# Optimization experiments

Hardware: AMD Instinct MI355X
Metric: run time of the kernel (lower is better)

## Reference

```python
import jax, jax.numpy as jnp
import numpy as np

K_TOP = 2  # top-k experts per token


def setup_inputs() -> dict:
    key = jax.random.key(0)
    k1, k2, k3 = jax.random.split(key, 3)
    B, S, H, E = 4, 2048, 1024, 8
    hidden_states = jax.random.normal(k1, (B, S, H), dtype=jnp.float32)
    router_w = jax.random.normal(k2, (E, H), dtype=jnp.float32) * 0.02
    expert_weights = jax.random.normal(k3, (E, H, H), dtype=jnp.float32) * 0.02
    return {"hidden_states": hidden_states, "router_w": router_w, "expert_weights": expert_weights}


def reference(hidden_states, router_w, expert_weights):
    B, S, H = hidden_states.shape
    x = hidden_states.reshape(-1, H)                      # [N, H], N = B*S
    logits = x @ router_w.T                               # [N, E]
    probs = jax.nn.softmax(logits, axis=-1)               # [N, E]
    topk_vals, topk_idx = jax.lax.top_k(probs, K_TOP)     # [N, K]
    topk_w = topk_vals / (topk_vals.sum(-1, keepdims=True) + 1e-6)  # [N, K]

    # Dense per-expert GEMM over all tokens (single-device dispatch = identity)
    expert_out = jnp.einsum('nh,eho->eno', x, expert_weights)  # [E, N, H]

    # all_to_all_combine: gather each token's K expert outputs
    combined = jnp.take_along_axis(
        expert_out.transpose(1, 0, 2),                    # [N, E, H]
        topk_idx[:, :, None], axis=1)                     # [N, K, H]
    combined = combined.transpose(1, 0, 2)                # [K, N, H]

    # remap bias: sum over last dim of one-hot(topk_idx) * router_prob == gathered prob
    remap_bias = jnp.take_along_axis(probs, topk_idx, axis=1).T[:, :, None]  # [K, N, 1]

    weights = topk_w.T[:, :, None]                        # [K, N, 1]
    out = ((combined + remap_bias) * weights).sum(axis=0) # [N, H]
    return out.reshape(B, S, H)
```

## Files before the change

kernel.cpp:

```cpp
#include <hip/hip_runtime.h>
#include <hip/hip_fp16.h>
#include <cstdint>

typedef unsigned short u16;
typedef __attribute__((ext_vector_type(8))) short short8;
typedef __attribute__((ext_vector_type(4))) float float4v;

#define NTOK 8192
#define HDIM 1024
#define NEXP 8
#define HTILE (128 * 64)
#define NITF 8
#define MAXT256 72
#define FATT 64
#define TMT 128
#define BKT 32
#define NITT (HDIM / BKT)
#define LAT (TMT * BKT)
#define WBLK 2048
#define RBLK 2048

__device__ __forceinline__ u16 f2bf(float f) {
    union { float f; uint32_t u; } v; v.f = f;
    uint32_t u = v.u;
    return (u16)((u + 0x7FFFu + ((u >> 16) & 1u)) >> 16);
}

__device__ __forceinline__ void gll16(const u16* g, u16* l) {
    __builtin_amdgcn_global_load_lds(
        (const __attribute__((address_space(1))) uint32_t*)g,
        (__attribute__((address_space(3))) uint32_t*)l,
        16, 0, 0);
}

__global__ __launch_bounds__(256) void prep(const float* __restrict__ x,
                                            const float* __restrict__ rw,
                                            const float* __restrict__ ew,
                                            u16* __restrict__ x_bf,
                                            u16* __restrict__ w_bf,
                                            float* __restrict__ wt0,
                                            float* __restrict__ wt1,
                                            float* __restrict__ biasv,
                                            int* __restrict__ sel,
                                            int* __restrict__ ctrl) {
    if (blockIdx.x == 0 && threadIdx.x < 132) ctrl[threadIdx.x] = 0;

    if (blockIdx.x < WBLK) {
        __shared__ float tile[64][65];
        const int bid = blockIdx.x;
        const int e  = bid >> 8;
        const int k0 = ((bid >> 4) & 15) * 64;
        const int n0 = (bid & 15) * 64;
        const int kr = threadIdx.x >> 2;
        const int ng = (threadIdx.x & 3) * 16;
        const float* src = ew + ((size_t)e << 20) + (size_t)(k0 + kr) * HDIM + n0 + ng;
#pragma unroll
        for (int j = 0; j < 4; j++) {
            const float4 v = *(const float4*)(src + 4 * j);
            tile[kr][ng + 4*j]     = v.x;
            tile[kr][ng + 4*j + 1] = v.y;
            tile[kr][ng + 4*j + 2] = v.z;
            tile[kr][ng + 4*j + 3] = v.w;
        }
        __syncthreads();
        const int nr = threadIdx.x >> 2;
        const int kg = (threadIdx.x & 3) * 16;
        u16* dst = w_bf + ((size_t)e << 20) + (size_t)(n0 + nr) * HDIM + k0 + kg;
#pragma unroll
        for (int j = 0; j < 4; j++) {
            ushort4 o;
            o.x = f2bf(tile[kg + 4*j][nr]);
            o.y = f2bf(tile[kg + 4*j + 1][nr]);
            o.z = f2bf(tile[kg + 4*j + 2][nr]);
            o.w = f2bf(tile[kg + 4*j + 3][nr]);
            *(ushort4*)(dst + 4 * j) = o;
        }
    } else {
        const int wv = threadIdx.x >> 6;
        const int l  = threadIdx.x & 63;
        const int n  = (blockIdx.x - WBLK) * 4 + wv;
        const float4* xr = (const float4*)(x + (size_t)n * HDIM);
        ushort4* xo = (ushort4*)(x_bf + (size_t)n * HDIM);

        float4 xv[4];
#pragma unroll
        for (int t = 0; t < 4; t++) {
            xv[t] = xr[t * 64 + l];
            ushort4 p;
            p.x = f2bf(xv[t].x); p.y = f2bf(xv[t].y);
            p.z = f2bf(xv[t].z); p.w = f2bf(xv[t].w);
            xo[t * 64 + l] = p;
        }

        float logits[NEXP];
#pragma unroll
        for (int e = 0; e < NEXP; e++) {
            const float4* rwe = (const float4*)(rw + e * HDIM);
            float acc = 0.f;
#pragma unroll
            for (int t = 0; t < 4; t++) {
                const float4 r = rwe[t * 64 + l];
                acc += xv[t].x * r.x + xv[t].y * r.y + xv[t].z * r.z + xv[t].w * r.w;
            }
#pragma unroll
            for (int s = 32; s > 0; s >>= 1) acc += __shfl_xor(acc, s, 64);
            logits[e] = acc;
        }

        if (l == 0) {
            float mx = logits[0];
#pragma unroll
            for (int e = 1; e < NEXP; e++) mx = fmaxf(mx, logits[e]);
            float p[NEXP]; float sum = 0.f;
#pragma unroll
            for (int e = 0; e < NEXP; e++) { p[e] = expf(logits[e] - mx); sum += p[e]; }
            const float inv = 1.f / sum;
#pragma unroll
            for (int e = 0; e < NEXP; e++) p[e] *= inv;
            int e0 = 0;
#pragma unroll
            for (int e = 1; e < NEXP; e++) if (p[e] > p[e0]) e0 = e;
            int e1 = (e0 == 0) ? 1 : 0;
#pragma unroll
            for (int e = 0; e < NEXP; e++) if (e != e0 && p[e] > p[e1]) e1 = e;
            const float p0 = p[e0], p1 = p[e1];
            const float wsum = p0 + p1 + 1e-6f;
            const float w0 = p0 / wsum, w1 = p1 / wsum;
            wt0[n] = w0; wt1[n] = w1;
            biasv[n] = w0 * p0 + w1 * p1;
            sel[n] = e0 | (e1 << 8);
        }
    }
}

__global__ __launch_bounds__(256) void build_lists(const int* __restrict__ sel,
                                                   int* __restrict__ lists,
                                                   int* __restrict__ ctrl,
                                                   int* __restrict__ tmap,
                                                   int* __restrict__ tmap128) {
    const int n  = blockIdx.x * 256 + threadIdx.x;
    const int wv = threadIdx.x >> 6;
    const int l  = threadIdx.x & 63;
    const int s  = sel[n];
    const int e0 = s & 0xFF, e1 = s >> 8;
    __shared__ int wcnt[NEXP][4];
    __shared__ int ebase[NEXP];
    int pf0 = 0, pf1 = 0;
    const unsigned long long ltmask = (1ULL << l) - 1ULL;
#pragma unroll
    for (int e = 0; e < NEXP; e++) {
        const int slot = (e0 == e) ? 0 : ((e1 == e) ? 1 : -1);
        const unsigned long long bal = __ballot(slot >= 0);
        const int pf = __popcll(bal & ltmask);
        if (slot == 0) pf0 = pf;
        if (slot == 1) pf1 = pf;
        if (l == 0) wcnt[e][wv] = __popcll(bal);
    }
    __syncthreads();
    if (threadIdx.x < NEXP) {
        const int e = threadIdx.x;
        const int tot = wcnt[e][0] + wcnt[e][1] + wcnt[e][2] + wcnt[e][3];
        ebase[e] = atomicAdd(&ctrl[e * 16], tot);
    }
    __syncthreads();
    int off0 = ebase[e0], off1 = ebase[e1];
#pragma unroll
    for (int i = 0; i < 4; i++) {
        off0 += (i < wv) ? wcnt[e0][i] : 0;
        off1 += (i < wv) ? wcnt[e1][i] : 0;
    }
    lists[e0 * NTOK + off0 + pf0] = n;
    lists[e1 * NTOK + off1 + pf1] = n | 0x10000;

    __shared__ int lastflag;
    __threadfence();
    if (threadIdx.x == 0) lastflag = (atomicAdd(&ctrl[128], 1) == (int)gridDim.x - 1);
    __syncthreads();
    if (lastflag) {
        __shared__ int tbase[NEXP + 1];
        __shared__ int cnts[NEXP];
        if (threadIdx.x == 0) {
            int acc = 0;
            for (int e = 0; e < NEXP; e++) {
                tbase[e] = acc;
                cnts[e] = atomicAdd(&ctrl[e * 16], 0);
                acc += (cnts[e] + 255) / 256;
            }
            tbase[NEXP] = acc;
        }
        __syncthreads();
        for (int i = threadIdx.x; i < MAXT256; i += 256) {
            int v = -1;
#pragma unroll
            for (int e = 0; e < NEXP; e++)
                if (i >= tbase[e] && i < tbase[e + 1]) v = (e << 16) | (i - tbase[e]);
            tmap[i] = v;
        }
        if (threadIdx.x < 16) {
            const int j = threadIdx.x;
            const int i256 = FATT + (j >> 1);
            int v = -1;
            if (i256 < tbase[NEXP]) {
                int ve = 0;
#pragma unroll
                for (int e = 0; e < NEXP; e++)
                    if (i256 >= tbase[e] && i256 < tbase[e + 1]) ve = e;
                const int m256 = i256 - tbase[ve];
                const int m128 = m256 * 2 + (j & 1);
                if (m128 * 128 < cnts[ve]) v = (ve << 16) | m128;
            }
            tmap128[j] = v;
        }
    }
}

__global__ __launch_bounds__(512, 2) void moe_gemm_fat(const u16* __restrict__ x_bf,
                                                       const u16* __restrict__ wt_bf,
                                                       const int* __restrict__ lists,
                                                       const int* __restrict__ ctrl,
                                                       const int* __restrict__ tmap,
                                                       const float* __restrict__ wt0,
                                                       const float* __restrict__ wt1,
                                                       const float* __restrict__ biasv,
                                                       __half* __restrict__ stage0,
                                                       __half* __restrict__ stage1) {
    const int ent = tmap[blockIdx.x];
    if (ent < 0) return;
    const int e = ent >> 16;
    const int tile_m = (ent & 0xFFFF) * 256;
    const int cnt = ctrl[e * 16];
    const int tn = blockIdx.y * 256;

    __shared__ u16 lA[4 * HTILE];
    __shared__ u16 lB[4 * HTILE];
    __shared__ int   toks[256];
    __shared__ float wgt[256];
    __shared__ float bia[256];
    __shared__ int   slt[256];

    const int t  = threadIdx.x;
    const int wv = t >> 6;
    const int l  = t & 63;

    if (t < 256) {
        const int idx = tile_m + t;
        int tok = 0; float w = 0.f, b = 0.f; int sl = 0;
        if (idx < cnt) {
            const int entry = lists[e * NTOK + idx];
            tok = entry & 0xFFFF;
            sl = entry >> 16;
            w = sl ? wt1[tok] : wt0[tok];
            b = sl ? 0.f : biasv[tok];
        }
        toks[t] = tok; wgt[t] = w; bia[t] = b; slt[t] = sl;
    }
    __syncthreads();

    const u16* const wbase = wt_bf + ((size_t)e << 20);
    const u16* pA[2][2]; const u16* pB[2][2];
    int dst0, dst1;
    {
        const int s0 = (0 * 8 + wv) * 64 + l;
        const int s1 = (1 * 8 + wv) * 64 + l;
        const int r0 = s0 >> 3, r1 = s1 >> 3;
        const int g0s = (s0 & 7) ^ (r0 & 7);
        const int g1s = (s1 & 7) ^ (r1 & 7);
        dst0 = (0 * 8 + wv) * 512;
        dst1 = (1 * 8 + wv) * 512;
#pragma unroll
        for (int h = 0; h < 2; h++) {
            pA[0][h] = x_bf + (size_t)toks[h * 128 + r0] * HDIM + g0s * 8;
            pA[1][h] = x_bf + (size_t)toks[h * 128 + r1] * HDIM + g1s * 8;
            pB[0][h] = wbase + (size_t)(tn + h * 128 + r0) * HDIM + g0s * 8;
            pB[1][h] = wbase + (size_t)(tn + h * 128 + r1) * HDIM + g1s * 8;
        }
    }

#define STAGE_A(par, h, ktile) do { \
    gll16(pA[0][h] + (ktile) * 64, lA + (par) * 2 * HTILE + (h) * HTILE + dst0); \
    gll16(pA[1][h] + (ktile) * 64, lA + (par) * 2 * HTILE + (h) * HTILE + dst1); } while (0)
#define STAGE_B(par, h, ktile) do { \
    gll16(pB[0][h] + (ktile) * 64, lB + (par) * 2 * HTILE + (h) * HTILE + dst0); \
    gll16(pB[1][h] + (ktile) * 64, lB + (par) * 2 * HTILE + (h) * HTILE + dst1); } while (0)

    const int wm2 = wv >> 2;
    const int wn4 = wv & 3;
    const int fm = l & 15;
    const int fq = l >> 4;
    const int f7 = fm & 7;
    const int pg0 = ((0 + fq) ^ f7) * 8;
    const int pg1 = ((4 + fq) ^ f7) * 8;
    const int arow = fm * 64;
    const int brow = (wn4 & 1) * 4096 + fm * 64;
    const u16* const Abase = lA + wm2 * HTILE;
    const u16* const Bbase = lB + (wn4 >> 1) * HTILE;

    short8 afr[4][2];
    short8 bfr[2][2][2];

#define LDA_H(par, mq) do { \
    _Pragma("unroll") \
    for (int mfL = 0; mfL < 4; mfL++) { \
        afr[mfL][0] = *(const short8*)(Abase + (par) * 2 * HTILE + ((mq) * 4 + mfL) * 1024 + arow + pg0); \
        afr[mfL][1] = *(const short8*)(Abase + (par) * 2 * HTILE + ((mq) * 4 + mfL) * 1024 + arow + pg1); \
    } } while (0)
#define LDB_H(par, nq) do { \
    _Pragma("unroll") \
    for (int nfL = 0; nfL < 2; nfL++) { \
        bfr[nq][nfL][0] = *(const short8*)(Bbase + (par) * 2 * HTILE + ((nq) * 2 + nfL) * 1024 + brow + pg0); \
        bfr[nq][nfL][1] = *(const short8*)(Bbase + (par) * 2 * HTILE + ((nq) * 2 + nfL) * 1024 + brow + pg1); \
    } } while (0)

    float4v acc[8][4];
#pragma unroll
    for (int i = 0; i < 8; i++)
#pragma unroll
        for (int j = 0; j < 4; j++) { float4v z = {0.f, 0.f, 0.f, 0.f}; acc[i][j] = z; }

#define MFMA_Q(mq, nq) do { \
    __builtin_amdgcn_s_setprio(1); \
    _Pragma("unroll") \
    for (int ks = 0; ks < 2; ks++) \
    _Pragma("unroll") \
    for (int mfL = 0; mfL < 4; mfL++) \
    _Pragma("unroll") \
    for (int nfL = 0; nfL < 2; nfL++) \
        acc[(mq) * 4 + mfL][(nq) * 2 + nfL] = __builtin_amdgcn_mfma_f32_16x16x32_bf16( \
            afr[mfL][ks], bfr[nq][nfL][ks], acc[(mq) * 4 + mfL][(nq) * 2 + nfL], 0, 0, 0); \
    __builtin_amdgcn_s_setprio(0); } while (0)

#define BARx() __builtin_amdgcn_s_barrier()
#define LGKM0 do { asm volatile("s_waitcnt lgkmcnt(0)" ::: "memory"); \
                   __builtin_amdgcn_sched_barrier(0); } while (0)
#define VM2 asm volatile("s_waitcnt vmcnt(2)" ::: "memory")
#define VM0 asm volatile("s_waitcnt vmcnt(0)" ::: "memory")

    STAGE_A(0, 0, 0); STAGE_A(0, 1, 0);
    STAGE_B(0, 0, 0); STAGE_B(0, 1, 0);
    STAGE_A(1, 0, 1);
    VM0; BARx();

#pragma unroll
    for (int it = 0; it < NITF; ++it) {
        const bool st = (it < NITF - 1);
        LDA_H(0, 0); LDB_H(0, 0);
        STAGE_A(1, 1, 2 * it + 1);
        BARx(); LGKM0;
        MFMA_Q(0, 0);
        BARx();
        LDB_H(0, 1);
        STAGE_B(1, 0, 2 * it + 1);
        BARx(); LGKM0;
        MFMA_Q(0, 1);
        BARx();
        LDA_H(0, 1);
        STAGE_B(1, 1, 2 * it + 1);
        BARx(); LGKM0;
        MFMA_Q(1, 1);
        BARx();
        if (st) STAGE_A(0, 0, 2 * it + 2);
        BARx();
        MFMA_Q(1, 0);
        if (st) { VM2; } else { VM0; }
        BARx();
        LDA_H(1, 0); LDB_H(1, 0);
        if (st) STAGE_A(0, 1, 2 * it + 2);
        BARx(); LGKM0;
        MFMA_Q(0, 0);
        BARx();
        LDB_H(1, 1);
        if (st) STAGE_B(0, 0, 2 * it + 2);
        BARx(); LGKM0;
        MFMA_Q(0, 1);
        BARx();
        LDA_H(1, 1);
        if (st) STAGE_B(0, 1, 2 * it + 2);
        BARx(); LGKM0;
        MFMA_Q(1, 1);
        BARx();
        if (st) STAGE_A(1, 0, 2 * it + 3);
        BARx();
        MFMA_Q(1, 0);
        if (st) { VM2; } else { VM0; }
        BARx();
    }

#pragma unroll
    for (int mf = 0; mf < 8; mf++) {
#pragma unroll
        for (int r = 0; r < 4; r++) {
            const int m_local = wm2 * 128 + mf * 16 + fq * 4 + r;
            if (tile_m + m_local < cnt) {
                const int tok = toks[m_local];
                const float w = wgt[m_local], b = bia[m_local];
                __half* sp = (slt[m_local] ? stage1 : stage0) + (size_t)tok * HDIM;
#pragma unroll
                for (int nf = 0; nf < 4; nf++) {
                    const int h = tn + wn4 * 64 + nf * 16 + fm;
                    sp[h] = __float2half(acc[mf][nf][r] * w + b);
                }
            }
        }
    }
#undef STAGE_A
#undef STAGE_B
#undef LDA_H
#undef LDB_H
#undef MFMA_Q
#undef BARx
#undef LGKM0
#undef VM2
#undef VM0
}

__global__ __launch_bounds__(256, 3) void moe_gemm_thin(const u16* __restrict__ x_bf,
                                                        const u16* __restrict__ wt_bf,
                                                        const int* __restrict__ lists,
                                                        const int* __restrict__ ctrl,
                                                        const int* __restrict__ tmap128,
                                                        const float* __restrict__ wt0,
                                                        const float* __restrict__ wt1,
                                                        const float* __restrict__ biasv,
                                                        __half* __restrict__ stage0,
                                                        __half* __restrict__ stage1) {
    const int ent = tmap128[blockIdx.x];
    if (ent < 0) return;
    const int e = ent >> 16;
    const int tile_m = (ent & 0xFFFF) * TMT;
    const int cnt = ctrl[e * 16];
    const int tn = blockIdx.y * TMT;

    __shared__ u16 lA[3 * LAT];
    __shared__ u16 lB[3 * LAT];
    __shared__ int   toks[TMT];
    __shared__ float wgt[TMT];
    __shared__ float bia[TMT];
    __shared__ int   slt[TMT];

    const int t  = threadIdx.x;
    const int wv = t >> 6;
    const int l  = t & 63;

    if (t < TMT) {
        const int idx = tile_m + t;
        int tok = 0; float w = 0.f, b = 0.f; int sl = 0;
        if (idx < cnt) {
            const int entry = lists[e * NTOK + idx];
            tok = entry & 0xFFFF;
            sl = entry >> 16;
            w = sl ? wt1[tok] : wt0[tok];
            b = sl ? 0.f : biasv[tok];
        }
        toks[t] = tok; wgt[t] = w; bia[t] = b; slt[t] = sl;
    }
    __syncthreads();

    const u16* gA[2]; const u16* gB[2]; int dAB[2];
#pragma unroll
    for (int i = 0; i < 2; i++) {
        const int slot = (i * 4 + wv) * 64 + l;
        const int row  = slot >> 2;
        const int c    = (slot & 3) ^ ((row >> 1) & 3);
        gA[i] = x_bf + (size_t)toks[row] * HDIM + c * 8;
        gB[i] = wt_bf + ((size_t)e << 20) + (size_t)(tn + row) * HDIM + c * 8;
        dAB[i] = (i * 4 + wv) * 512;
    }

    const int wm = (wv & 1) * 64;
    const int wn = (wv >> 1) * 64;
    const int fm = l & 15;
    const int fq = l >> 4;
    int aoff[4], boff[4];
#pragma unroll
    for (int i = 0; i < 4; i++) {
        const int ra = wm + i * 16 + fm;
        const int rb = wn + i * 16 + fm;
        aoff[i] = ra * BKT + ((fq ^ ((ra >> 1) & 3)) * 8);
        boff[i] = rb * BKT + ((fq ^ ((rb >> 1) & 3)) * 8);
    }

    float4v acc[4][4];
#pragma unroll
    for (int i = 0; i < 4; i++)
#pragma unroll
        for (int j = 0; j < 4; j++) { float4v z = {0.f, 0.f, 0.f, 0.f}; acc[i][j] = z; }

    short8 afr[2][4], bfr[2][4];

#pragma unroll
    for (int tk = 0; tk < 3; tk++) {
#pragma unroll
        for (int i = 0; i < 2; i++) {
            gll16(gA[i] + tk * BKT, lA + tk * LAT + dAB[i]);
            gll16(gB[i] + tk * BKT, lB + tk * LAT + dAB[i]);
        }
    }
    asm volatile("s_waitcnt vmcnt(8)\n\ts_barrier" ::: "memory");
#pragma unroll
    for (int i = 0; i < 4; i++) {
        afr[0][i] = *(const short8*)&lA[aoff[i]];
        bfr[0][i] = *(const short8*)&lB[boff[i]];
    }

#pragma unroll
    for (int it = 0; it < NITT; ++it) {
        const int cs = it & 1;
        const int ns = cs ^ 1;

        if (it == 0) {
            asm volatile("s_waitcnt vmcnt(4)\n\ts_barrier" ::: "memory");
        } else if (it < NITT - 1) {
            asm volatile("s_waitcnt vmcnt(0)\n\ts_barrier" ::: "memory");
        }

        if (it >= 1 && it + 2 < NITT) {
            const int nb = (it + 2) % 3;
            const int nk = (it + 2) * BKT;
#pragma unroll
            for (int i = 0; i < 2; i++) {
                gll16(gA[i] + nk, lA + nb * LAT + dAB[i]);
                gll16(gB[i] + nk, lB + nb * LAT + dAB[i]);
            }
        }

        if (it + 1 < NITT) {
            const u16* ca = lA + ((it + 1) % 3) * LAT;
            const u16* cb = lB + ((it + 1) % 3) * LAT;
#pragma unroll
            for (int i = 0; i < 4; i++) {
                afr[ns][i] = *(const short8*)&ca[aoff[i]];
                bfr[ns][i] = *(const short8*)&cb[boff[i]];
            }
            asm volatile("s_waitcnt lgkmcnt(8)" ::: "memory");
        } else {
            asm volatile("s_waitcnt lgkmcnt(0)" ::: "memory");
        }
        __builtin_amdgcn_sched_barrier(0);

        __builtin_amdgcn_s_setprio(1);
#pragma unroll
        for (int i = 0; i < 4; i++)
#pragma unroll
            for (int nf = 0; nf < 4; nf++)
                acc[i][nf] = __builtin_amdgcn_mfma_f32_16x16x32_bf16(
                    afr[cs][i], bfr[cs][nf], acc[i][nf], 0, 0, 0);
        __builtin_amdgcn_s_setprio(0);
    }

#pragma unroll
    for (int mf = 0; mf < 4; mf++) {
#pragma unroll
        for (int r = 0; r < 4; r++) {
            const int m_local = wm + mf * 16 + fq * 4 + r;
            if (tile_m + m_local < cnt) {
                const int tok = toks[m_local];
                const float w = wgt[m_local], b = bia[m_local];
                __half* sp = (slt[m_local] ? stage1 : stage0) + (size_t)tok * HDIM;
#pragma unroll
                for (int nf = 0; nf < 4; nf++) {
                    const int h = tn + wn + nf * 16 + fm;
                    sp[h] = __float2half(acc[mf][nf][r] * w + b);
                }
            }
        }
    }
}

__global__ __launch_bounds__(256) void combine(const __half* __restrict__ s0,
                                               const __half* __restrict__ s1,
                                               float* __restrict__ out) {
    const size_t idx = ((size_t)blockIdx.x * 256 + threadIdx.x) * 8;
    union { uint4 v; __half h[8]; } a, b;
    a.v = *(const uint4*)(s0 + idx);
    b.v = *(const uint4*)(s1 + idx);
    float4 o0, o1;
    o0.x = __half2float(a.h[0]) + __half2float(b.h[0]);
    o0.y = __half2float(a.h[1]) + __half2float(b.h[1]);
    o0.z = __half2float(a.h[2]) + __half2float(b.h[2]);
    o0.w = __half2float(a.h[3]) + __half2float(b.h[3]);
    o1.x = __half2float(a.h[4]) + __half2float(b.h[4]);
    o1.y = __half2float(a.h[5]) + __half2float(b.h[5]);
    o1.z = __half2float(a.h[6]) + __half2float(b.h[6]);
    o1.w = __half2float(a.h[7]) + __half2float(b.h[7]);
    *(float4*)(out + idx)     = o0;
    *(float4*)(out + idx + 4) = o1;
}

extern "C" void kernel_launch(void* const* d_in, const int* in_sizes, int n_in,
                              void* d_out, int out_size, void* d_ws, size_t ws_size,
                              hipStream_t stream) {
    const float* x  = (const float*)d_in[0];
    const float* rw = (const float*)d_in[1];
    const float* ew = (const float*)d_in[2];
    float* out = (float*)d_out;

    char* ws = (char*)d_ws;
    u16*    x_bf    = (u16*)ws;
    u16*    w_bf    = (u16*)(ws + 16777216);
    __half* stage0  = (__half*)(ws + 33554432);
    __half* stage1  = (__half*)(ws + 50331648);
    float*  wt0     = (float*)(ws + 67108864);
    float*  wt1     = (float*)(ws + 67141632);
    float*  biasv   = (float*)(ws + 67174400);
    int*    sel     = (int*)(ws + 67207168);
    int*    lists   = (int*)(ws + 67239936);
    int*    ctrl    = (int*)(ws + 67502080);
    int*    tmap    = (int*)(ws + 67502720);
    int*    tmap128 = (int*)(ws + 67503104);

    prep<<<WBLK + RBLK, 256, 0, stream>>>(x, rw, ew, x_bf, w_bf, wt0, wt1, biasv, sel, ctrl);
    build_lists<<<NTOK / 256, 256, 0, stream>>>(sel, lists, ctrl, tmap, tmap128);
    moe_gemm_fat<<<dim3(FATT, 4, 1), 512, 0, stream>>>(
        x_bf, w_bf, lists, ctrl, tmap, wt0, wt1, biasv, stage0, stage1);
    moe_gemm_thin<<<dim3(16, 8, 1), 256, 0, stream>>>(
        x_bf, w_bf, lists, ctrl, tmap128, wt0, wt1, biasv, stage0, stage1);
    combine<<<(NTOK * HDIM) / (256 * 8), 256, 0, stream>>>(stage0, stage1, out);
}
```

Baseline: 198.2 us.

## Split-K the thin tail GEMM and remap fat GEMM block order

The thin tail GEMM is split along K into four slices via blockIdx.z. Slice 0 writes to the staging buffers and the other slices write fp16 partials, which a new combine_tail kernel adds back into the staging rows. This is meant to fill the GPU during the small tail GEMM. The fat GEMM also linearizes its block index and permutes the tile/column mapping, likely to improve L2 locality or XCD distribution. The cost is an extra kernel launch, extra partial-sum traffic, and precision loss from summing fp16 partials.

Result: faster. 189.6 us (-4.3%).

```diff
diff --git a/kernel.cpp b/kernel.cpp
--- a/kernel.cpp
+++ b/kernel.cpp
@@ -15,8 +15,10 @@
 #define FATT 64
 #define TMT 128
 #define BKT 32
-#define NITT (HDIM / BKT)
+#define KST 4
+#define NITT (HDIM / BKT / KST)
 #define LAT (TMT * BKT)
+#define LROWS 2048
 #define WBLK 2048
 #define RBLK 2048
 
@@ -224,12 +226,16 @@
                                                        const float* __restrict__ biasv,
                                                        __half* __restrict__ stage0,
                                                        __half* __restrict__ stage1) {
-    const int ent = tmap[blockIdx.x];
+    const int bid = blockIdx.x + FATT * blockIdx.y;
+    const int li  = bid >> 3;
+    const int tile_idx = (bid & 7) * 8 + (li & 7);
+    const int quad     = li >> 3;
+    const int ent = tmap[tile_idx];
     if (ent < 0) return;
     const int e = ent >> 16;
     const int tile_m = (ent & 0xFFFF) * 256;
     const int cnt = ctrl[e * 16];
-    const int tn = blockIdx.y * 256;
+    const int tn = quad * 256;
 
     __shared__ u16 lA[4 * HTILE];
     __shared__ u16 lB[4 * HTILE];
@@ -422,13 +428,16 @@
                                                         const float* __restrict__ wt1,
                                                         const float* __restrict__ biasv,
                                                         __half* __restrict__ stage0,
-                                                        __half* __restrict__ stage1) {
+                                                        __half* __restrict__ stage1,
+                                                        __half* __restrict__ part) {
     const int ent = tmap128[blockIdx.x];
     if (ent < 0) return;
     const int e = ent >> 16;
     const int tile_m = (ent & 0xFFFF) * TMT;
     const int cnt = ctrl[e * 16];
     const int tn = blockIdx.y * TMT;
+    const int kz = blockIdx.z;
+    const int koff = kz * (HDIM / KST);
 
     __shared__ u16 lA[3 * LAT];
     __shared__ u16 lB[3 * LAT];
@@ -449,7 +458,7 @@
             tok = entry & 0xFFFF;
             sl = entry >> 16;
             w = sl ? wt1[tok] : wt0[tok];
-            b = sl ? 0.f : biasv[tok];
+            b = (sl || kz) ? 0.f : biasv[tok];
         }
         toks[t] = tok; wgt[t] = w; bia[t] = b; slt[t] = sl;
     }
@@ -461,8 +470,8 @@
         const int slot = (i * 4 + wv) * 64 + l;
         const int row  = slot >> 2;
         const int c    = (slot & 3) ^ ((row >> 1) & 3);
-        gA[i] = x_bf + (size_t)toks[row] * HDIM + c * 8;
-        gB[i] = wt_bf + ((size_t)e << 20) + (size_t)(tn + row) * HDIM + c * 8;
+        gA[i] = x_bf + (size_t)toks[row] * HDIM + koff + c * 8;
+        gB[i] = wt_bf + ((size_t)e << 20) + (size_t)(tn + row) * HDIM + koff + c * 8;
         dAB[i] = (i * 4 + wv) * 512;
     }
 
@@ -553,9 +562,13 @@
         for (int r = 0; r < 4; r++) {
             const int m_local = wm + mf * 16 + fq * 4 + r;
             if (tile_m + m_local < cnt) {
-                const int tok = toks[m_local];
                 const float w = wgt[m_local], b = bia[m_local];
-                __half* sp = (slt[m_local] ? stage1 : stage0) + (size_t)tok * HDIM;
+                __half* sp;
+                if (kz == 0) {
+                    sp = (slt[m_local] ? stage1 : stage0) + (size_t)toks[m_local] * HDIM;
+                } else {
+                    sp = part + ((size_t)(kz - 1) * LROWS + blockIdx.x * TMT + m_local) * HDIM;
+                }
 #pragma unroll
                 for (int nf = 0; nf < 4; nf++) {
                     const int h = tn + wn + nf * 16 + fm;
@@ -564,6 +577,35 @@
             }
         }
     }
+}
+
+__global__ __launch_bounds__(256) void combine_tail(const int* __restrict__ lists,
+                                                    const int* __restrict__ ctrl,
+                                                    const int* __restrict__ tmap128,
+                                                    const __half* __restrict__ part,
+                                                    __half* __restrict__ stage0,
+                                                    __half* __restrict__ stage1) {
+    const int r = blockIdx.x;
+    const int ent = tmap128[r >> 7];
+    if (ent < 0) return;
+    const int e = ent >> 16;
+    const int idx = (ent & 0xFFFF) * TMT + (r & 127);
+    if (idx >= ctrl[e * 16]) return;
+    const int entry = lists[e * NTOK + idx];
+    const int tok = entry & 0xFFFF;
+    __half* sp = ((entry >> 16) ? stage1 : stage0) + (size_t)tok * HDIM;
+    const __half* pp = part + (size_t)r * HDIM;
+    const int h = threadIdx.x * 4;
+    union U { ushort4 v; __half x[4]; } s, p0, p1, p2, o;
+    s.v  = *(const ushort4*)(sp + h);
+    p0.v = *(const ushort4*)(pp + h);
+    p1.v = *(const ushort4*)(pp + (size_t)LROWS * HDIM + h);
+    p2.v = *(const ushort4*)(pp + (size_t)2 * LROWS * HDIM + h);
+#pragma unroll
+    for (int i = 0; i < 4; i++)
+        o.x[i] = __float2half(__half2float(s.x[i]) + __half2float(p0.x[i]) +
+                              __half2float(p1.x[i]) + __half2float(p2.x[i]));
+    *(ushort4*)(sp + h) = o.v;
 }
 
 __global__ __launch_bounds__(256) void combine(const __half* __restrict__ s0,
@@ -607,12 +649,14 @@
     int*    ctrl    = (int*)(ws + 67502080);
     int*    tmap    = (int*)(ws + 67502720);
     int*    tmap128 = (int*)(ws + 67503104);
+    __half* part    = (__half*)(ws + 67512320);
 
     prep<<<WBLK + RBLK, 256, 0, stream>>>(x, rw, ew, x_bf, w_bf, wt0, wt1, biasv, sel, ctrl);
     build_lists<<<NTOK / 256, 256, 0, stream>>>(sel, lists, ctrl, tmap, tmap128);
     moe_gemm_fat<<<dim3(FATT, 4, 1), 512, 0, stream>>>(
         x_bf, w_bf, lists, ctrl, tmap, wt0, wt1, biasv, stage0, stage1);
-    moe_gemm_thin<<<dim3(16, 8, 1), 256, 0, stream>>>(
-        x_bf, w_bf, lists, ctrl, tmap128, wt0, wt1, biasv, stage0, stage1);
+    moe_gemm_thin<<<dim3(16, 8, KST), 256, 0, stream>>>(
+        x_bf, w_bf, lists, ctrl, tmap128, wt0, wt1, biasv, stage0, stage1, part);
+    combine_tail<<<LROWS, 256, 0, stream>>>(lists, ctrl, tmap128, part, stage0, stage1);
     combine<<<(NTOK * HDIM) / (256 * 8), 256, 0, stream>>>(stage0, stage1, out);
 }
```
